# Performance work log

Measured on AMD Instinct MI355X. Metric: run time of the kernel, lower is better.

Reference implementation:

```python
import jax, jax.numpy as jnp
import numpy as np

K = 20  # hard-coded neighbor count in the original module


def setup_inputs() -> dict:
    key = jax.random.key(0)
    ks = jax.random.split(key, 7)
    B, C, N = 16, 3, 4096
    return {
        "x": jax.random.normal(ks[0], (B, C, N), dtype=jnp.float32),
        "w1": jax.random.normal(ks[1], (16, 3), dtype=jnp.float32) * 0.3,
        "b1": jax.random.normal(ks[2], (16,), dtype=jnp.float32) * 0.1,
        "w2": jax.random.normal(ks[3], (16, 3), dtype=jnp.float32) * 0.3,
        "b2": jax.random.normal(ks[4], (16,), dtype=jnp.float32) * 0.1,
        "w3": jax.random.normal(ks[5], (1, 16), dtype=jnp.float32) * 0.3,
        "b3": jax.random.normal(ks[6], (1,), dtype=jnp.float32) * 0.1,
    }


def reference(x, w1, b1, w2, b2, w3, b3):
    # x: [B, 3, N]
    B, C, N = x.shape
    xt = jnp.transpose(x, (0, 2, 1))  # [B, N, 3]

    # --- KNN: topk of negative squared pairwise distance (includes self) ---
    xx = jnp.sum(x * x, axis=1)                      # [B, N]
    inner = jnp.einsum('bcn,bcm->bnm', x, x)         # [B, N, N]
    neg_dist = -xx[:, :, None] + 2.0 * inner - xx[:, None, :]
    _, idx = jax.lax.top_k(neg_dist, K)              # [B, N, K]

    # --- neighbor gather ---
    neighbors = jnp.take_along_axis(xt[:, None, :, :], idx[..., None], axis=2)  # [B,N,K,3]
    diff = xt[:, :, None, :] - neighbors             # [B, N, K, 3] (center - neighbor)

    # --- 1x1 conv branches (pointwise matmuls) ---
    f1 = jnp.einsum('bnc,oc->bno', xt, w1) + b1      # conv2d1: [B, N, 16]
    sa = jnp.einsum('bno,po->bnp', f1, w3) + b3      # conv2d3(self): [B, N, 1]
    x1 = jnp.einsum('bnkc,oc->bnko', diff, w2) + b2  # conv2d2: [B, N, K, 16]
    na = jnp.einsum('bnko,o->bnk', x1, w3[0]) + b3[0]  # conv2d3(edge): [B, N, K]

    # --- attention coefficients + aggregation ---
    logits = sa + na                                  # [B, N, K] (sa broadcasts over K)
    coefs = jax.nn.softmax(jax.nn.leaky_relu(logits, 0.01), axis=-1)
    vals = jnp.einsum('bnk,bnko->bno', coefs, x1)     # [B, N, 16]
    ret = jax.nn.elu(vals)
    return jnp.transpose(ret, (0, 2, 1))              # [B, 16, N]
```

## Files before the change

kernel.cpp:

```cpp
#include <hip/hip_runtime.h>
#include <math.h>
#include <float.h>

#define NPTS 4096
#define KNN  20
#define ROWSB 16

#define ROW_SHR1    0x111
#define ROW_SHR2    0x112
#define ROW_SHR4    0x114
#define ROW_SHR8    0x118
#define ROW_BCAST15 0x142
#define ROW_BCAST31 0x143

template <int CTRL>
__device__ __forceinline__ float dpp_mv(float x, float ident) {
    int r = __builtin_amdgcn_update_dpp(__float_as_int(ident), __float_as_int(x),
                                        CTRL, 0xf, 0xf, false);
    return __int_as_float(r);
}
__device__ __forceinline__ float readlane_f(float v, int l) {
    return __int_as_float(__builtin_amdgcn_readlane(__float_as_int(v), l));
}
__device__ __forceinline__ float wave_min_bcast(float v) {
    v = fminf(v, dpp_mv<ROW_SHR1>(v, FLT_MAX));
    v = fminf(v, dpp_mv<ROW_SHR2>(v, FLT_MAX));
    v = fminf(v, dpp_mv<ROW_SHR4>(v, FLT_MAX));
    v = fminf(v, dpp_mv<ROW_SHR8>(v, FLT_MAX));
    v = fminf(v, dpp_mv<ROW_BCAST15>(v, FLT_MAX));
    v = fminf(v, dpp_mv<ROW_BCAST31>(v, FLT_MAX));
    return readlane_f(v, 63);
}
__device__ __forceinline__ float half_max(float v) {
    v = fmaxf(v, dpp_mv<ROW_SHR1>(v, -FLT_MAX));
    v = fmaxf(v, dpp_mv<ROW_SHR2>(v, -FLT_MAX));
    v = fmaxf(v, dpp_mv<ROW_SHR4>(v, -FLT_MAX));
    v = fmaxf(v, dpp_mv<ROW_SHR8>(v, -FLT_MAX));
    v = fmaxf(v, dpp_mv<ROW_BCAST15>(v, -FLT_MAX));
    return v;
}
__device__ __forceinline__ float half_sum(float v) {
    v += dpp_mv<ROW_SHR1>(v, 0.f);
    v += dpp_mv<ROW_SHR2>(v, 0.f);
    v += dpp_mv<ROW_SHR4>(v, 0.f);
    v += dpp_mv<ROW_SHR8>(v, 0.f);
    v += dpp_mv<ROW_BCAST15>(v, 0.f);
    return v;
}

#define INS_STAGE(cc, ii)                                        \
    { bool lt_ = (v < cc);                                       \
      float mx_ = lt_ ? cc : v;  int mi_ = lt_ ? ii : vi;        \
      cc = lt_ ? v : cc;         ii = lt_ ? vi : ii;             \
      v = mx_; vi = mi_; }

#define REFILL(Q0,J0,Q1,J1,Q2,J2,Q3,J3,CX,CY,CZ,XX,ROW,T)               \
    {   Q0=FLT_MAX;Q1=FLT_MAX;Q2=FLT_MAX;Q3=FLT_MAX;                    \
        J0=-1;J1=-1;J2=-1;J3=-1;                                        \
        for (int j_ = 0; j_ < 64; ++j_) {                               \
            int m_ = (j_ << 6) + lane;                                  \
            bool ex_ = false;                                           \
            for (int e_ = 0; e_ <= T; ++e_) ex_ = ex_ || (s_nbr[ROW][e_] == m_); \
            if (!ex_) {                                                 \
                float mx2 = sc[m_], my2 = sc[m_+NPTS], mz2 = sc[m_+2*NPTS]; \
                float inner = CX*mx2 + CY*my2 + CZ*mz2;                 \
                float mxx2  = mx2*mx2 + my2*my2 + mz2*mz2;              \
                float v = mxx2 - (2.0f * inner - XX);                   \
                int vi = m_;                                            \
                INS_STAGE(Q0,J0) INS_STAGE(Q1,J1) INS_STAGE(Q2,J2) INS_STAGE(Q3,J3) \
            }                                                           \
        }                                                               \
    }

__global__ __launch_bounds__(512, 6)
void lae_kernel(const float* __restrict__ x,
                const float* __restrict__ w1, const float* __restrict__ b1,
                const float* __restrict__ w2, const float* __restrict__ b2,
                const float* __restrict__ w3, const float* __restrict__ b3,
                float* __restrict__ out)
{
    __shared__ float sc[3 * NPTS];
    __shared__ int   s_nbr[ROWSB][KNN];

    const int tid  = threadIdx.x;
    const int lane = tid & 63;
    const int wid  = tid >> 6;
    const int b    = blockIdx.y;
    const int rA   = blockIdx.x * ROWSB + wid * 2;
    const int rB   = rA + 1;

    const float* xb = x + (size_t)b * 3 * NPTS;
    #pragma unroll
    for (int i = tid; i < 3 * NPTS / 4; i += 512)
        ((float4*)sc)[i] = ((const float4*)xb)[i];
    __syncthreads();

    const float cxA = sc[rA], cyA = sc[rA + NPTS], czA = sc[rA + 2*NPTS];
    const float cxB = sc[rB], cyB = sc[rB + NPTS], czB = sc[rB + 2*NPTS];
    const float xxA = cxA*cxA + cyA*cyA + czA*czA;
    const float xxB = cxB*cxB + cyB*cyB + czB*czB;

    float qA0=FLT_MAX,qA1=FLT_MAX,qA2=FLT_MAX,qA3=FLT_MAX;
    int   jA0=-1,jA1=-1,jA2=-1,jA3=-1;
    float qB0=FLT_MAX,qB1=FLT_MAX,qB2=FLT_MAX,qB3=FLT_MAX;
    int   jB0=-1,jB1=-1,jB2=-1,jB3=-1;

    float nx = sc[lane], ny = sc[lane + NPTS], nz = sc[lane + 2*NPTS];
    #pragma unroll 2
    for (int j = 0; j < 64; ++j) {
        const int mi = (j << 6) + lane;
        const float mx = nx, my = ny, mz = nz;
        const int mn = (mi + 64) & (NPTS - 1);
        nx = sc[mn]; ny = sc[mn + NPTS]; nz = sc[mn + 2*NPTS];
        const float mxx = mx*mx + my*my + mz*mz;
        {
            float inner = cxA*mx + cyA*my + czA*mz;
            float v = mxx - (2.0f * inner - xxA);
            int vi = mi;
            INS_STAGE(qA0,jA0) INS_STAGE(qA1,jA1) INS_STAGE(qA2,jA2) INS_STAGE(qA3,jA3)
        }
        {
            float inner = cxB*mx + cyB*my + czB*mz;
            float v = mxx - (2.0f * inner - xxB);
            int vi = mi;
            INS_STAGE(qB0,jB0) INS_STAGE(qB1,jB1) INS_STAGE(qB2,jB2) INS_STAGE(qB3,jB3)
        }
    }

    int cntA = 4, cntB = 4;
    for (int t = 0; t < KNN; ++t) {
        float gA = wave_min_bcast(qA0);
        float gB = wave_min_bcast(qB0);
        unsigned long long mkA = __ballot(qA0 == gA);
        unsigned long long mkB = __ballot(qB0 == gB);
        int wA = (int)__builtin_ctzll(mkA);
        int wB = (int)__builtin_ctzll(mkB);
        int mA = __builtin_amdgcn_readlane(jA0, wA);
        int mB = __builtin_amdgcn_readlane(jB0, wB);
        if (lane == 0) { s_nbr[wid*2][t] = mA; s_nbr[wid*2+1][t] = mB; }
        if (lane == wA) {
            qA0=qA1; jA0=jA1; qA1=qA2; jA1=jA2; qA2=qA3; jA2=jA3;
            qA3=FLT_MAX; jA3=-1; cntA--;
        }
        if (lane == wB) {
            qB0=qB1; jB0=jB1; qB1=qB2; jB1=jB2; qB2=qB3; jB2=jB3;
            qB3=FLT_MAX; jB3=-1; cntB--;
        }
        if (cntA == 0) { REFILL(qA0,jA0,qA1,jA1,qA2,jA2,qA3,jA3,cxA,cyA,czA,xxA,wid*2,t)   cntA = 4; }
        if (cntB == 0) { REFILL(qB0,jB0,qB1,jB1,qB2,jB2,qB3,jB3,cxB,cyB,czB,xxB,wid*2+1,t) cntB = 4; }
    }

    const int  kh    = lane & 31;
    const bool lower = (lane < 32);
    const float ex = lower ? cxA : cxB;
    const float ey = lower ? cyA : cyB;
    const float ez = lower ? czA : czB;
    const int rowInBlk = wid*2 + (lower ? 0 : 1);
    const int nrow = lower ? rA : rB;

    float sa = b3[0];
    #pragma unroll
    for (int o = 0; o < 16; ++o) {
        float f = b1[o] + w1[o*3+0]*ex + w1[o*3+1]*ey + w1[o*3+2]*ez;
        sa += w3[o] * f;
    }

    const int kk = (kh < KNN) ? kh : 0;
    const int m = s_nbr[rowInBlk][kk];
    float dx = ex - sc[m], dy = ey - sc[m + NPTS], dz = ez - sc[m + 2*NPTS];
    float x1v[16];
    float na = b3[0];
    #pragma unroll
    for (int o = 0; o < 16; ++o) {
        float t2 = b2[o] + w2[o*3+0]*dx + w2[o*3+1]*dy + w2[o*3+2]*dz;
        x1v[o] = t2;
        na += w3[o] * t2;
    }
    float logit = sa + na;
    float l = (logit >= 0.f) ? logit : 0.01f * logit;
    const bool valid = (kh < KNN);

    float hm  = half_max(valid ? l : -FLT_MAX);
    float lm  = lower ? readlane_f(hm, 31) : readlane_f(hm, 63);
    float p   = valid ? expf(l - lm) : 0.f;
    float hs  = half_sum(p);
    float ps  = lower ? readlane_f(hs, 31) : readlane_f(hs, 63);
    float coef = p / ps;

    float res = 0.f;
    #pragma unroll
    for (int o = 0; o < 16; ++o) {
        float s  = half_sum(coef * x1v[o]);
        float sv = lower ? readlane_f(s, 31) : readlane_f(s, 63);
        res = (kh == o) ? sv : res;
    }
    if (kh < 16) {
        float r = (res > 0.f) ? res : expm1f(res);
        out[((size_t)b * 16 + kh) * NPTS + nrow] = r;
    }
}

extern "C" void kernel_launch(void* const* d_in, const int* in_sizes, int n_in,
                              void* d_out, int out_size, void* d_ws, size_t ws_size,
                              hipStream_t stream)
{
    const float* x  = (const float*)d_in[0];
    const float* w1 = (const float*)d_in[1];
    const float* b1 = (const float*)d_in[2];
    const float* w2 = (const float*)d_in[3];
    const float* b2 = (const float*)d_in[4];
    const float* w3 = (const float*)d_in[5];
    const float* b3 = (const float*)d_in[6];
    float* out = (float*)d_out;

    dim3 grid(NPTS / ROWSB, 16, 1);
    lae_kernel<<<grid, dim3(512, 1, 1), 0, stream>>>(x, w1, b1, w2, b2, w3, b3, out);
}
```

Measured before the change: 400.5 us.

## Process four query rows per wave with float4 candidate loads from LDS

Each wave now handles four query rows instead of two, so every candidate point loaded from shared memory feeds four distance/insertion computations. The candidate scan reads float4 vectors, so each lane covers four contiguous points per chunk instead of strided single loads. The aim is to cut LDS traffic per distance and halve the number of blocks. In exchange, per-thread register state doubles, which can lower occupancy, and the refill path is serialized per row.

```diff
diff --git a/kernel.cpp b/kernel.cpp
--- a/kernel.cpp
+++ b/kernel.cpp
@@ -4,7 +4,10 @@
 
 #define NPTS 4096
 #define KNN  20
-#define ROWSB 16
+#define RPW  4
+#define WAVES 8
+#define ROWSB (WAVES * RPW)
+#define NCHUNK (NPTS / 256)
 
 #define ROW_SHR1    0x111
 #define ROW_SHR2    0x112
@@ -54,23 +57,8 @@
       cc = lt_ ? v : cc;         ii = lt_ ? vi : ii;             \
       v = mx_; vi = mi_; }
 
-#define REFILL(Q0,J0,Q1,J1,Q2,J2,Q3,J3,CX,CY,CZ,XX,ROW,T)               \
-    {   Q0=FLT_MAX;Q1=FLT_MAX;Q2=FLT_MAX;Q3=FLT_MAX;                    \
-        J0=-1;J1=-1;J2=-1;J3=-1;                                        \
-        for (int j_ = 0; j_ < 64; ++j_) {                               \
-            int m_ = (j_ << 6) + lane;                                  \
-            bool ex_ = false;                                           \
-            for (int e_ = 0; e_ <= T; ++e_) ex_ = ex_ || (s_nbr[ROW][e_] == m_); \
-            if (!ex_) {                                                 \
-                float mx2 = sc[m_], my2 = sc[m_+NPTS], mz2 = sc[m_+2*NPTS]; \
-                float inner = CX*mx2 + CY*my2 + CZ*mz2;                 \
-                float mxx2  = mx2*mx2 + my2*my2 + mz2*mz2;              \
-                float v = mxx2 - (2.0f * inner - XX);                   \
-                int vi = m_;                                            \
-                INS_STAGE(Q0,J0) INS_STAGE(Q1,J1) INS_STAGE(Q2,J2) INS_STAGE(Q3,J3) \
-            }                                                           \
-        }                                                               \
-    }
+#define INS4(R)  INS_STAGE(q[R][0], ji[R][0]) INS_STAGE(q[R][1], ji[R][1]) \
+                 INS_STAGE(q[R][2], ji[R][2]) INS_STAGE(q[R][3], ji[R][3])
 
 __global__ __launch_bounds__(512, 6)
 void lae_kernel(const float* __restrict__ x,
@@ -79,15 +67,14 @@
                 const float* __restrict__ w3, const float* __restrict__ b3,
                 float* __restrict__ out)
 {
-    __shared__ float sc[3 * NPTS];
-    __shared__ int   s_nbr[ROWSB][KNN];
+    __shared__ __align__(16) float sc[3 * NPTS];
+    __shared__ int s_nbr[ROWSB][KNN];
 
     const int tid  = threadIdx.x;
     const int lane = tid & 63;
     const int wid  = tid >> 6;
     const int b    = blockIdx.y;
-    const int rA   = blockIdx.x * ROWSB + wid * 2;
-    const int rB   = rA + 1;
+    const int rbase = blockIdx.x * ROWSB + wid * RPW;
 
     const float* xb = x + (size_t)b * 3 * NPTS;
     #pragma unroll
@@ -95,108 +82,155 @@
         ((float4*)sc)[i] = ((const float4*)xb)[i];
     __syncthreads();
 
-    const float cxA = sc[rA], cyA = sc[rA + NPTS], czA = sc[rA + 2*NPTS];
-    const float cxB = sc[rB], cyB = sc[rB + NPTS], czB = sc[rB + 2*NPTS];
-    const float xxA = cxA*cxA + cyA*cyA + czA*czA;
-    const float xxB = cxB*cxB + cyB*cyB + czB*czB;
-
-    float qA0=FLT_MAX,qA1=FLT_MAX,qA2=FLT_MAX,qA3=FLT_MAX;
-    int   jA0=-1,jA1=-1,jA2=-1,jA3=-1;
-    float qB0=FLT_MAX,qB1=FLT_MAX,qB2=FLT_MAX,qB3=FLT_MAX;
-    int   jB0=-1,jB1=-1,jB2=-1,jB3=-1;
-
-    float nx = sc[lane], ny = sc[lane + NPTS], nz = sc[lane + 2*NPTS];
-    #pragma unroll 2
-    for (int j = 0; j < 64; ++j) {
-        const int mi = (j << 6) + lane;
-        const float mx = nx, my = ny, mz = nz;
-        const int mn = (mi + 64) & (NPTS - 1);
-        nx = sc[mn]; ny = sc[mn + NPTS]; nz = sc[mn + 2*NPTS];
-        const float mxx = mx*mx + my*my + mz*mz;
-        {
-            float inner = cxA*mx + cyA*my + czA*mz;
-            float v = mxx - (2.0f * inner - xxA);
-            int vi = mi;
-            INS_STAGE(qA0,jA0) INS_STAGE(qA1,jA1) INS_STAGE(qA2,jA2) INS_STAGE(qA3,jA3)
-        }
-        {
-            float inner = cxB*mx + cyB*my + czB*mz;
-            float v = mxx - (2.0f * inner - xxB);
-            int vi = mi;
-            INS_STAGE(qB0,jB0) INS_STAGE(qB1,jB1) INS_STAGE(qB2,jB2) INS_STAGE(qB3,jB3)
-        }
-    }
-
-    int cntA = 4, cntB = 4;
+    float cx[RPW], cy[RPW], cz[RPW], xx[RPW];
+    #pragma unroll
+    for (int r = 0; r < RPW; ++r) {
+        cx[r] = sc[rbase + r];
+        cy[r] = sc[rbase + r + NPTS];
+        cz[r] = sc[rbase + r + 2 * NPTS];
+        xx[r] = cx[r]*cx[r] + cy[r]*cy[r] + cz[r]*cz[r];
+    }
+
+    float q[RPW][4];
+    int   ji[RPW][4];
+    #pragma unroll
+    for (int r = 0; r < RPW; ++r)
+        #pragma unroll
+        for (int s = 0; s < 4; ++s) { q[r][s] = FLT_MAX; ji[r][s] = -1; }
+
+    const float4* s4 = (const float4*)sc;
+
+    for (int ch = 0; ch < NCHUNK; ++ch) {
+        const int f4i = (ch << 6) + lane;
+        float px[4], py[4], pz[4];
+        *(float4*)px = s4[f4i];
+        *(float4*)py = s4[f4i + 1024];
+        *(float4*)pz = s4[f4i + 2048];
+        const int mbase = (ch << 8) + (lane << 2);
+        #pragma unroll
+        for (int c = 0; c < 4; ++c) {
+            const float mx = px[c], my = py[c], mz = pz[c];
+            const float mxx = mx*mx + my*my + mz*mz;
+            const int mi = mbase + c;
+            #pragma unroll
+            for (int r = 0; r < RPW; ++r) {
+                float inner = cx[r]*mx + cy[r]*my + cz[r]*mz;
+                float v = mxx - (2.0f * inner - xx[r]);
+                int vi = mi;
+                INS4(r)
+            }
+        }
+    }
+
+    int cnt[RPW] = {4, 4, 4, 4};
     for (int t = 0; t < KNN; ++t) {
-        float gA = wave_min_bcast(qA0);
-        float gB = wave_min_bcast(qB0);
-        unsigned long long mkA = __ballot(qA0 == gA);
-        unsigned long long mkB = __ballot(qB0 == gB);
-        int wA = (int)__builtin_ctzll(mkA);
-        int wB = (int)__builtin_ctzll(mkB);
-        int mA = __builtin_amdgcn_readlane(jA0, wA);
-        int mB = __builtin_amdgcn_readlane(jB0, wB);
-        if (lane == 0) { s_nbr[wid*2][t] = mA; s_nbr[wid*2+1][t] = mB; }
-        if (lane == wA) {
-            qA0=qA1; jA0=jA1; qA1=qA2; jA1=jA2; qA2=qA3; jA2=jA3;
-            qA3=FLT_MAX; jA3=-1; cntA--;
-        }
-        if (lane == wB) {
-            qB0=qB1; jB0=jB1; qB1=qB2; jB1=jB2; qB2=qB3; jB2=jB3;
-            qB3=FLT_MAX; jB3=-1; cntB--;
-        }
-        if (cntA == 0) { REFILL(qA0,jA0,qA1,jA1,qA2,jA2,qA3,jA3,cxA,cyA,czA,xxA,wid*2,t)   cntA = 4; }
-        if (cntB == 0) { REFILL(qB0,jB0,qB1,jB1,qB2,jB2,qB3,jB3,cxB,cyB,czB,xxB,wid*2+1,t) cntB = 4; }
+        float g[RPW]; int win[RPW]; int midx[RPW];
+        #pragma unroll
+        for (int r = 0; r < RPW; ++r) g[r] = wave_min_bcast(q[r][0]);
+        #pragma unroll
+        for (int r = 0; r < RPW; ++r) {
+            unsigned long long mk = __ballot(q[r][0] == g[r]);
+            win[r]  = (int)__builtin_ctzll(mk);
+            midx[r] = __builtin_amdgcn_readlane(ji[r][0], win[r]);
+        }
+        if (lane == 0) {
+            #pragma unroll
+            for (int r = 0; r < RPW; ++r) s_nbr[wid * RPW + r][t] = midx[r];
+        }
+        #pragma unroll
+        for (int r = 0; r < RPW; ++r) {
+            if (lane == win[r]) {
+                q[r][0] = q[r][1]; ji[r][0] = ji[r][1];
+                q[r][1] = q[r][2]; ji[r][1] = ji[r][2];
+                q[r][2] = q[r][3]; ji[r][2] = ji[r][3];
+                q[r][3] = FLT_MAX; ji[r][3] = -1;
+                cnt[r]--;
+            }
+        }
+        #pragma unroll
+        for (int r = 0; r < RPW; ++r) {
+            if (cnt[r] == 0) {
+                q[r][0] = FLT_MAX; q[r][1] = FLT_MAX; q[r][2] = FLT_MAX; q[r][3] = FLT_MAX;
+                ji[r][0] = -1; ji[r][1] = -1; ji[r][2] = -1; ji[r][3] = -1;
+                for (int ch = 0; ch < NCHUNK; ++ch) {
+                    const int f4i = (ch << 6) + lane;
+                    float px[4], py[4], pz[4];
+                    *(float4*)px = s4[f4i];
+                    *(float4*)py = s4[f4i + 1024];
+                    *(float4*)pz = s4[f4i + 2048];
+                    const int mbase = (ch << 8) + (lane << 2);
+                    #pragma unroll
+                    for (int c = 0; c < 4; ++c) {
+                        const int mi = mbase + c;
+                        bool ex = false;
+                        for (int e = 0; e <= t; ++e)
+                            ex = ex || (s_nbr[wid * RPW + r][e] == mi);
+                        if (!ex) {
+                            const float mx = px[c], my = py[c], mz = pz[c];
+                            float inner = cx[r]*mx + cy[r]*my + cz[r]*mz;
+                            float mxx   = mx*mx + my*my + mz*mz;
+                            float v = mxx - (2.0f * inner - xx[r]);
+                            int vi = mi;
+                            INS4(r)
+                        }
+                    }
+                }
+                cnt[r] = 4;
+            }
+        }
     }
 
     const int  kh    = lane & 31;
     const bool lower = (lane < 32);
-    const float ex = lower ? cxA : cxB;
-    const float ey = lower ? cyA : cyB;
-    const float ez = lower ? czA : czB;
-    const int rowInBlk = wid*2 + (lower ? 0 : 1);
-    const int nrow = lower ? rA : rB;
-
-    float sa = b3[0];
-    #pragma unroll
-    for (int o = 0; o < 16; ++o) {
-        float f = b1[o] + w1[o*3+0]*ex + w1[o*3+1]*ey + w1[o*3+2]*ez;
-        sa += w3[o] * f;
-    }
-
-    const int kk = (kh < KNN) ? kh : 0;
-    const int m = s_nbr[rowInBlk][kk];
-    float dx = ex - sc[m], dy = ey - sc[m + NPTS], dz = ez - sc[m + 2*NPTS];
-    float x1v[16];
-    float na = b3[0];
-    #pragma unroll
-    for (int o = 0; o < 16; ++o) {
-        float t2 = b2[o] + w2[o*3+0]*dx + w2[o*3+1]*dy + w2[o*3+2]*dz;
-        x1v[o] = t2;
-        na += w3[o] * t2;
-    }
-    float logit = sa + na;
-    float l = (logit >= 0.f) ? logit : 0.01f * logit;
     const bool valid = (kh < KNN);
-
-    float hm  = half_max(valid ? l : -FLT_MAX);
-    float lm  = lower ? readlane_f(hm, 31) : readlane_f(hm, 63);
-    float p   = valid ? expf(l - lm) : 0.f;
-    float hs  = half_sum(p);
-    float ps  = lower ? readlane_f(hs, 31) : readlane_f(hs, 63);
-    float coef = p / ps;
-
-    float res = 0.f;
-    #pragma unroll
-    for (int o = 0; o < 16; ++o) {
-        float s  = half_sum(coef * x1v[o]);
-        float sv = lower ? readlane_f(s, 31) : readlane_f(s, 63);
-        res = (kh == o) ? sv : res;
-    }
-    if (kh < 16) {
-        float r = (res > 0.f) ? res : expm1f(res);
-        out[((size_t)b * 16 + kh) * NPTS + nrow] = r;
+    const int  kk    = valid ? kh : 0;
+
+    #pragma unroll
+    for (int p = 0; p < 2; ++p) {
+        const float ex = lower ? cx[2*p] : cx[2*p+1];
+        const float ey = lower ? cy[2*p] : cy[2*p+1];
+        const float ez = lower ? cz[2*p] : cz[2*p+1];
+        const int rib  = wid * RPW + 2*p + (lower ? 0 : 1);
+        const int nrow = rbase + 2*p + (lower ? 0 : 1);
+
+        float sa = b3[0];
+        #pragma unroll
+        for (int o = 0; o < 16; ++o) {
+            float f = b1[o] + w1[o*3+0]*ex + w1[o*3+1]*ey + w1[o*3+2]*ez;
+            sa += w3[o] * f;
+        }
+
+        const int m = s_nbr[rib][kk];
+        float dx = ex - sc[m], dy = ey - sc[m + NPTS], dz = ez - sc[m + 2*NPTS];
+        float x1v[16];
+        float na = b3[0];
+        #pragma unroll
+        for (int o = 0; o < 16; ++o) {
+            float t2 = b2[o] + w2[o*3+0]*dx + w2[o*3+1]*dy + w2[o*3+2]*dz;
+            x1v[o] = t2;
+            na += w3[o] * t2;
+        }
+        float logit = sa + na;
+        float l = (logit >= 0.f) ? logit : 0.01f * logit;
+
+        float hm  = half_max(valid ? l : -FLT_MAX);
+        float lm  = lower ? readlane_f(hm, 31) : readlane_f(hm, 63);
+        float pr  = valid ? expf(l - lm) : 0.f;
+        float hs  = half_sum(pr);
+        float ps  = lower ? readlane_f(hs, 31) : readlane_f(hs, 63);
+        float coef = pr / ps;
+
+        float res = 0.f;
+        #pragma unroll
+        for (int o = 0; o < 16; ++o) {
+            float s  = half_sum(coef * x1v[o]);
+            float sv = lower ? readlane_f(s, 31) : readlane_f(s, 63);
+            res = (kh == o) ? sv : res;
+        }
+        if (kh < 16) {
+            float r2 = (res > 0.f) ? res : expm1f(res);
+            out[((size_t)b * 16 + kh) * NPTS + nrow] = r2;
+        }
     }
 }
 
```

Measured after the change: 417.4 us. 1.04x slower.
